# Kernel tuning notes

Hardware: AMD Instinct MI355X
Metric: run time of the kernel (lower is better)

The kernel has to match this reference:

```python
import jax, jax.numpy as jnp
import numpy as np

D = 512       # d_model
M = 64        # working memory_dim
SE = 32       # episodic slots
SS = 64       # semantic slots
H = 4         # episodic heads
B, L = 2, 1024
BOT = max(D // 4, 32)  # controller bottleneck = 128


def _layernorm(x, g, b, eps=1e-5):
    mu = jnp.mean(x, axis=-1, keepdims=True)
    var = jnp.var(x, axis=-1, keepdims=True)
    return (x - mu) * jax.lax.rsqrt(var + eps) * g + b


def setup_inputs() -> dict:
    key = jax.random.key(0)
    ks = jax.random.split(key, 24)
    r = lambda i, shape, s=0.02: jax.random.normal(ks[i], shape, dtype=jnp.float32) * s
    return {
        "x": jax.random.normal(ks[0], (B, L, D), dtype=jnp.float32),
        # WorkingMemory (weights stored as (in, out))
        "Wq": r(1, (D, M)), "Wk": r(2, (D, M)), "Wv": r(3, (D, D)),
        "Wf": r(4, (D, M)), "bf": jnp.zeros((M,), jnp.float32),
        "Wo": r(5, (D, D)),
        "ln_g": jnp.ones((D,), jnp.float32), "ln_b": jnp.zeros((D,), jnp.float32),
        # EpisodicMemory
        "eslots": r(6, (1, SE, D)),
        "Eq": r(7, (D, D)), "Ek": r(8, (D, D)), "Ev": r(9, (D, D)), "Eo": r(10, (D, D)),
        # SemanticMemory
        "know": r(11, (1, SS, D)),
        "Sin": r(12, (D, D)),
        "Sg_w": r(13, (D, D)), "Sg_b": jnp.zeros((D,), jnp.float32),
        "So": r(14, (D, D)),
        # MemoryController
        "C1w": r(15, (D, BOT)), "C1b": jnp.zeros((BOT,), jnp.float32),
        "C2w": r(16, (BOT, 3)), "C2b": jnp.zeros((3,), jnp.float32),
    }


def _forward(x, Wq, Wk, Wv, Wf, bf, Wo, ln_g, ln_b,
             eslots, Eq, Ek, Ev, Eo,
             know, Sin, Sg_w, Sg_b, So,
             C1w, C1b, C2w, C2b):
    b, l, d = x.shape
    # ---- WorkingMemory (parallel gated linear attention) ----
    scale = M ** -0.5
    q = (jax.nn.elu(x @ Wq) + 1.0) * scale          # (B,L,M)
    k = jax.nn.elu(x @ Wk) + 1.0                    # (B,L,M)
    v = x @ Wv                                      # (B,L,D)
    forget = jax.nn.sigmoid(x @ Wf + bf)            # (B,L,M)
    log_f_cum = jnp.clip(jnp.cumsum(jnp.log(jnp.clip(forget, 1e-6, None)), axis=1), -20.0, 20.0)
    exp_neg = jnp.exp(-log_f_cum)
    exp_pos = jnp.exp(log_f_cum)
    kv = k[..., :, None] * v[..., None, :]          # (B,L,M,D) outer product
    cum_kv = jnp.cumsum(exp_neg[..., None] * kv, axis=1)
    Mstate = exp_pos[..., None] * cum_kv            # (B,L,M,D)
    z = exp_pos * jnp.cumsum(exp_neg * k, axis=1)   # (B,L,M)
    num = jnp.einsum('blm,blmd->bld', q, Mstate)
    den = jnp.einsum('blm,blm->bl', q, z)[..., None] + 1e-6
    w_out = _layernorm(num / den, ln_g, ln_b) @ Wo  # (B,L,D)

    # ---- EpisodicMemory (cross-attn to learned slots) ----
    hd = D // H
    mem = jnp.broadcast_to(eslots, (b, SE, D))
    qh = (x @ Eq).reshape(b, l, H, hd)
    kh = (mem @ Ek).reshape(b, SE, H, hd)
    vh = (mem @ Ev).reshape(b, SE, H, hd)
    scores = jnp.einsum('blhe,bshe->bhls', qh, kh) / jnp.sqrt(jnp.float32(hd))
    attn = jax.nn.softmax(scores, axis=-1)
    e_out = jnp.einsum('bhls,bshe->blhe', attn, vh).reshape(b, l, D) @ Eo

    # ---- SemanticMemory (single-head attn to knowledge, gated residual) ----
    kb = jnp.broadcast_to(know, (b, SS, D))
    qs = x @ Sin                                    # (B,L,D)
    s_scores = jnp.einsum('bld,bsd->bls', qs, kb) / jnp.sqrt(jnp.float32(D))
    s_attn = jax.nn.softmax(s_scores, axis=-1)
    retrieved = jnp.einsum('bls,bsd->bld', s_attn, kb)
    gate = jax.nn.sigmoid(x @ Sg_w + Sg_b)
    s_out = (gate * retrieved + (1.0 - gate) * x) @ So

    # ---- Controller fusion ----
    wts = jax.nn.softmax(jax.nn.silu(x @ C1w + C1b) @ C2w + C2b, axis=-1)  # (B,L,3)
    fused = (wts[..., 0:1] * w_out + wts[..., 1:2] * e_out + wts[..., 2:3] * s_out)
    return fused


def reference(x, Wq, Wk, Wv, Wf, bf, Wo, ln_g, ln_b,
              eslots, Eq, Ek, Ev, Eo,
              know, Sin, Sg_w, Sg_b, So,
              C1w, C1b, C2w, C2b):
    return _forward(x, Wq, Wk, Wv, Wf, bf, Wo, ln_g, ln_b,
                    eslots, Eq, Ek, Ev, Eo,
                    know, Sin, Sg_w, Sg_b, So,
                    C1w, C1b, C2w, C2b)
```

## Files before the change

### kernel.cpp

```cpp
#include <hip/hip_runtime.h>
#include <cstdint>

typedef unsigned int uint;
typedef unsigned short ushort;
typedef __attribute__((ext_vector_type(8))) short bf16x8;
typedef __attribute__((ext_vector_type(4))) float f32x4;

__device__ __forceinline__ ushort f2b(float f) {
  union { float f; uint u; } v; v.f = f;
  uint u = v.u;
  uint r = (u + 0x7FFFu + ((u >> 16) & 1u)) >> 16;
  return (ushort)r;
}
__device__ __forceinline__ float b2f(ushort h) {
  union { uint u; float f; } v; v.u = ((uint)h) << 16; return v.f;
}

__global__ __launch_bounds__(256) void k_prep(
    const float* __restrict__ x, const float* __restrict__ Wv, const float* __restrict__ Sg,
    const float* __restrict__ C1w, const float* __restrict__ Wq, const float* __restrict__ Wk,
    const float* __restrict__ Wo, const float* __restrict__ So, const float* __restrict__ know,
    const float* __restrict__ eslots, const float* __restrict__ Ek, const float* __restrict__ Ev,
    const float* __restrict__ Sin, const float* __restrict__ Wf, const float* __restrict__ bfb,
    ushort* __restrict__ X16, ushort* __restrict__ Wcat, ushort* __restrict__ Wfin,
    ushort* __restrict__ know16, float* __restrict__ kh, float* __restrict__ vh,
    float* __restrict__ logfb)
{
  __shared__ __align__(16) float Af[16 * 32];
  __shared__ __align__(16) float Bf[32 * 64];
  __shared__ __align__(16) float T[64][65];
  int bid = blockIdx.x;
  int tid = threadIdx.x;
  int lane = tid & 63, wv = tid >> 6;

  if (bid < 128) {
    int r0 = bid * 16;
    int row = tid >> 4, col4 = (tid & 15) * 4;
    float a0 = 0.f, a1 = 0.f, a2 = 0.f, a3 = 0.f;
    for (int kt = 0; kt < 16; ++kt) {
      if (tid < 128) {
        int p = tid; int rr = p >> 3, c4 = (p & 7) * 4;
        *(float4*)&Af[rr * 32 + c4] = *(const float4*)&x[(size_t)(r0 + rr) * 512 + kt * 32 + c4];
      }
      #pragma unroll
      for (int i = 0; i < 2; ++i) {
        int p = i * 256 + tid; int rr = p >> 4, c4 = (p & 15) * 4;
        *(float4*)&Bf[rr * 64 + c4] = *(const float4*)&Wf[(size_t)(kt * 32 + rr) * 64 + c4];
      }
      __syncthreads();
      #pragma unroll 8
      for (int ks = 0; ks < 32; ++ks) {
        float a = Af[row * 32 + ks];
        float4 b = *(float4*)&Bf[ks * 64 + col4];
        a0 += a * b.x; a1 += a * b.y; a2 += a * b.z; a3 += a * b.w;
      }
      __syncthreads();
    }
    float accs[4] = {a0, a1, a2, a3};
    #pragma unroll
    for (int j = 0; j < 4; ++j) {
      float logit = accs[j] + bfb[col4 + j];
      float s = 1.f / (1.f + expf(-logit));
      logfb[(size_t)(r0 + row) * 64 + col4 + j] = logf(fmaxf(s, 1e-6f));
    }
    return;
  }
  if (bid < 256) {
    int t = (bid - 128) * 256 + tid;
    if (t < 16384) {
      int s = t >> 9, j = t & 511;
      float acc = 0.f;
      #pragma unroll 8
      for (int d = 0; d < 512; ++d) acc += eslots[s * 512 + d] * Ek[d * 512 + j];
      kh[s * 512 + j] = acc;
    } else {
      int o = t - 16384; int s = o >> 9, j = o & 511;
      float acc = 0.f;
      #pragma unroll 8
      for (int d = 0; d < 512; ++d) acc += eslots[s * 512 + d] * Ev[d * 512 + j];
      vh[s * 512 + j] = acc;
    }
    return;
  }
  if (bid < 384) {
    int k = (bid - 256) * 4 + wv;
    const float* sp = Sin + (size_t)k * 512 + lane * 8;
    float4 s1 = *(const float4*)&sp[0];
    float4 s2 = *(const float4*)&sp[4];
    for (int s = 0; s < 64; ++s) {
      const float* kp = know + (size_t)s * 512 + lane * 8;
      float4 k1 = *(const float4*)&kp[0];
      float4 k2 = *(const float4*)&kp[4];
      float part = s1.x * k1.x + s1.y * k1.y + s1.z * k1.z + s1.w * k1.w
                 + s2.x * k2.x + s2.y * k2.y + s2.z * k2.z + s2.w * k2.w;
      #pragma unroll
      for (int o = 32; o; o >>= 1) part += __shfl_xor(part, o);
      if (lane == 0) Wcat[(640 + s) * 512 + k] = f2b(part * 0.04419417382415922f);
    }
    return;
  }
  if (bid < 672) {
    int tt = bid - 384;
    const float* src; ushort* dst; int sld, dld, Nt, drow, dcol;
    if (tt < 64)       {           src = Wv;  dst = Wcat; sld = 512; dld = 512;  Nt = 8; drow = 0;    dcol = 0;   }
    else if (tt < 128) { tt -= 64; src = Sg;  dst = Wcat; sld = 512; dld = 512;  Nt = 8; drow = 704;  dcol = 0;   }
    else if (tt < 144) { tt -= 128; src = C1w; dst = Wcat; sld = 128; dld = 512; Nt = 2; drow = 1216; dcol = 0;   }
    else if (tt < 152) { tt -= 144; src = Wq;  dst = Wcat; sld = 64;  dld = 512; Nt = 1; drow = 1344; dcol = 0;   }
    else if (tt < 160) { tt -= 152; src = Wk;  dst = Wcat; sld = 64;  dld = 512; Nt = 1; drow = 1408; dcol = 0;   }
    else if (tt < 224) { tt -= 160; src = Wo;  dst = Wfin; sld = 512; dld = 1152; Nt = 8; drow = 0;   dcol = 0;   }
    else               { tt -= 224; src = So;  dst = Wfin; sld = 512; dld = 1152; Nt = 8; drow = 0;   dcol = 512; }
    int tk = tt / Nt, tn = tt % Nt;
    int k0 = tk * 64, n0 = tn * 64;
    int r = tid >> 4, c = (tid & 15) * 4;
    #pragma unroll
    for (int p = 0; p < 4; ++p) {
      int kk = p * 16 + r;
      float4 v = *(const float4*)&src[(size_t)(k0 + kk) * sld + n0 + c];
      T[c + 0][kk] = v.x; T[c + 1][kk] = v.y; T[c + 2][kk] = v.z; T[c + 3][kk] = v.w;
    }
    __syncthreads();
    int n = tid >> 2, kc = (tid & 3) * 16;
    uint u[8];
    #pragma unroll
    for (int j = 0; j < 8; ++j) {
      ushort lo = f2b(T[n][kc + 2 * j]);
      ushort hi = f2b(T[n][kc + 2 * j + 1]);
      u[j] = (uint)lo | ((uint)hi << 16);
    }
    size_t off = (size_t)(drow + n0 + n) * dld + dcol + k0 + kc;
    uint4 o1; o1.x = u[0]; o1.y = u[1]; o1.z = u[2]; o1.w = u[3];
    uint4 o2; o2.x = u[4]; o2.y = u[5]; o2.z = u[6]; o2.w = u[7];
    *(uint4*)&dst[off] = o1;
    *(uint4*)&dst[off + 8] = o2;
    return;
  }
  if (bid < 800) {
    int base = (bid - 672) * 256 + tid;
    #pragma unroll
    for (int it = 0; it < 8; ++it) {
      int t = base + it * 32768;
      float4 xv = *(const float4*)&x[(size_t)t * 4];
      uint2 o;
      o.x = (uint)f2b(xv.x) | ((uint)f2b(xv.y) << 16);
      o.y = (uint)f2b(xv.z) | ((uint)f2b(xv.w) << 16);
      *(uint2*)&X16[(size_t)t * 4] = o;
    }
    return;
  }
  {
    int t = (bid - 800) * 256 + tid;
    #pragma unroll
    for (int j = 0; j < 2; ++j) {
      float4 v = *(const float4*)&know[(size_t)t * 8 + j * 4];
      uint2 o;
      o.x = (uint)f2b(v.x) | ((uint)f2b(v.y) << 16);
      o.y = (uint)f2b(v.z) | ((uint)f2b(v.w) << 16);
      *(uint2*)&know16[(size_t)t * 8 + j * 4] = o;
    }
  }
}

__global__ __launch_bounds__(256) void k_pre2(
    const float* __restrict__ Eq, const float* __restrict__ kh, const float* __restrict__ vh,
    const float* __restrict__ Eo, ushort* __restrict__ Wcat, ushort* __restrict__ Wfin)
{
  int bid = blockIdx.x;
  int tid = threadIdx.x;
  int lane = tid & 63, wv = tid >> 6;
  if (bid < 256) {
    int gw = bid * 4 + wv;
    #pragma unroll
    for (int pp = 0; pp < 2; ++pp) {
      int pair = gw * 2 + pp;
      int k = pair >> 2, h = pair & 3;
      const float* ep = Eq + (size_t)k * 512 + h * 128 + lane * 2;
      float e0 = ep[0], e1 = ep[1];
      for (int s = 0; s < 32; ++s) {
        const float* kp = kh + (size_t)s * 512 + h * 128 + lane * 2;
        float part = e0 * kp[0] + e1 * kp[1];
        #pragma unroll
        for (int o = 32; o; o >>= 1) part += __shfl_xor(part, o);
        if (lane == 0) Wcat[(512 + h * 32 + s) * 512 + k] = f2b(part * 0.08838834764831845f);
      }
    }
  } else {
    int o = (bid - 256) * 256 + tid;
    int hs = o >> 9, j = o & 511;
    int h = hs >> 5, s = hs & 31;
    const float* vhp = vh + (size_t)s * 512 + h * 128;
    float acc = 0.f;
    #pragma unroll 8
    for (int e = 0; e < 128; ++e) acc += vhp[e] * Eo[(size_t)(h * 128 + e) * 512 + j];
    Wfin[(size_t)j * 1152 + 1024 + hs] = f2b(acc);
  }
}

__global__ __launch_bounds__(256) void k_gemm1(
    const ushort* __restrict__ A, const ushort* __restrict__ Bw, float* __restrict__ C,
    const float* __restrict__ sgb, const float* __restrict__ c1b)
{
  __shared__ __align__(16) ushort As[64 * 32];
  __shared__ __align__(16) ushort Bs[128 * 32];
  int tid = threadIdx.x;
  int lane = tid & 63, wv = tid >> 6;
  int wm = (wv & 1) * 32, wn = (wv >> 1) * 64;
  int lr = lane & 15, lk = lane >> 4;
  int m0 = blockIdx.y * 64, n0 = blockIdx.x * 128;
  f32x4 zero4 = {0.f, 0.f, 0.f, 0.f};
  f32x4 acc[2][4];
  #pragma unroll
  for (int a = 0; a < 2; ++a)
    #pragma unroll
    for (int b = 0; b < 4; ++b) acc[a][b] = zero4;
  for (int kt = 0; kt < 16; ++kt) {
    int k0 = kt * 32;
    {
      int p = tid, row = p >> 2, cc = p & 3;
      int cs = cc ^ ((row >> 1) & 3);
      *(uint4*)&As[p * 8] = *(const uint4*)&A[(size_t)(m0 + row) * 512 + k0 + cs * 8];
    }
    #pragma unroll
    for (int i = 0; i < 2; ++i) {
      int p = i * 256 + tid, row = p >> 2, cc = p & 3;
      int cs = cc ^ ((row >> 1) & 3);
      *(uint4*)&Bs[p * 8] = *(const uint4*)&Bw[(size_t)(n0 + row) * 512 + k0 + cs * 8];
    }
    __syncthreads();
    bf16x8 af[2], bfv[4];
    #pragma unroll
    for (int mi = 0; mi < 2; ++mi) {
      int row = wm + mi * 16 + lr;
      int cc = lk ^ ((row >> 1) & 3);
      af[mi] = *(bf16x8*)&As[row * 32 + cc * 8];
    }
    #pragma unroll
    for (int ni = 0; ni < 4; ++ni) {
      int row = wn + ni * 16 + lr;
      int cc = lk ^ ((row >> 1) & 3);
      bfv[ni] = *(bf16x8*)&Bs[row * 32 + cc * 8];
    }
    #pragma unroll
    for (int mi = 0; mi < 2; ++mi)
      #pragma unroll
      for (int ni = 0; ni < 4; ++ni)
        acc[mi][ni] = __builtin_amdgcn_mfma_f32_16x16x32_bf16(af[mi], bfv[ni], acc[mi][ni], 0, 0, 0);
    __syncthreads();
  }
  #pragma unroll
  for (int mi = 0; mi < 2; ++mi) {
    #pragma unroll
    for (int ni = 0; ni < 4; ++ni) {
      int col = n0 + wn + ni * 16 + lr;
      #pragma unroll
      for (int r = 0; r < 4; ++r) {
        int rowb = m0 + wm + mi * 16 + lk * 4 + r;
        float v = acc[mi][ni][r];
        if (col >= 704) {
          if (col < 1216) { v = 1.f / (1.f + __expf(-(v + sgb[col - 704]))); }
          else if (col < 1344) { float tt = v + c1b[col - 1216]; v = tt / (1.f + __expf(-tt)); }
          else if (col < 1408) { float e = (v > 0.f) ? v : (__expf(v) - 1.f); v = (e + 1.f) * 0.125f; }
          else if (col < 1472) { float e = (v > 0.f) ? v : (__expf(v) - 1.f); v = e + 1.f; }
        }
        C[(size_t)rowb * 1536 + col] = v;
      }
    }
  }
}

__global__ __launch_bounds__(256) void k_gemm2(
    const ushort* __restrict__ A, const ushort* __restrict__ Bw, float* __restrict__ C)
{
  __shared__ __align__(16) ushort As[64 * 32];
  __shared__ __align__(16) ushort Bs[64 * 32];
  int tid = threadIdx.x;
  int lane = tid & 63, wv = tid >> 6;
  int wm = (wv & 1) * 32, wn = (wv >> 1) * 32;
  int lr = lane & 15, lk = lane >> 4;
  int m0 = blockIdx.y * 64, n0 = blockIdx.x * 64;
  f32x4 zero4 = {0.f, 0.f, 0.f, 0.f};
  f32x4 acc[2][2];
  #pragma unroll
  for (int a = 0; a < 2; ++a)
    #pragma unroll
    for (int b = 0; b < 2; ++b) acc[a][b] = zero4;
  for (int kt = 0; kt < 36; ++kt) {
    int k0 = kt * 32;
    {
      int p = tid, row = p >> 2, cc = p & 3;
      int cs = cc ^ ((row >> 1) & 3);
      *(uint4*)&As[p * 8] = *(const uint4*)&A[(size_t)(m0 + row) * 1152 + k0 + cs * 8];
      *(uint4*)&Bs[p * 8] = *(const uint4*)&Bw[(size_t)(n0 + row) * 1152 + k0 + cs * 8];
    }
    __syncthreads();
    bf16x8 af[2], bfv[2];
    #pragma unroll
    for (int mi = 0; mi < 2; ++mi) {
      int row = wm + mi * 16 + lr;
      int cc = lk ^ ((row >> 1) & 3);
      af[mi] = *(bf16x8*)&As[row * 32 + cc * 8];
    }
    #pragma unroll
    for (int ni = 0; ni < 2; ++ni) {
      int row = wn + ni * 16 + lr;
      int cc = lk ^ ((row >> 1) & 3);
      bfv[ni] = *(bf16x8*)&Bs[row * 32 + cc * 8];
    }
    #pragma unroll
    for (int mi = 0; mi < 2; ++mi)
      #pragma unroll
      for (int ni = 0; ni < 2; ++ni)
        acc[mi][ni] = __builtin_amdgcn_mfma_f32_16x16x32_bf16(af[mi], bfv[ni], acc[mi][ni], 0, 0, 0);
    __syncthreads();
  }
  #pragma unroll
  for (int mi = 0; mi < 2; ++mi) {
    #pragma unroll
    for (int ni = 0; ni < 2; ++ni) {
      int col = n0 + wn + ni * 16 + lr;
      #pragma unroll
      for (int r = 0; r < 4; ++r) {
        int rowb = m0 + wm + mi * 16 + lk * 4 + r;
        C[(size_t)rowb * 512 + col] = acc[mi][ni][r];
      }
    }
  }
}

__global__ __launch_bounds__(256) void k_gatescan(
    const float* __restrict__ logfb, const float* __restrict__ P,
    float* __restrict__ cn, float* __restrict__ qe, float* __restrict__ qz)
{
  __shared__ float wsumA[4];
  __shared__ float wsumB[4];
  int bidx = blockIdx.x;
  int b = bidx >> 6, m = bidx & 63;
  int tid = threadIdx.x;
  int lane = tid & 63, wv = tid >> 6;
  size_t rbase = (size_t)b * 1024 + tid * 4;

  float v0 = logfb[(rbase + 0) * 64 + m];
  float v1 = logfb[(rbase + 1) * 64 + m];
  float v2 = logfb[(rbase + 2) * 64 + m];
  float v3 = logfb[(rbase + 3) * 64 + m];
  v1 += v0; v2 += v1; v3 += v2;
  float tsum = v3;
  float sc = tsum;
  #pragma unroll
  for (int o = 1; o < 64; o <<= 1) {
    float t = __shfl_up(sc, o, 64);
    if (lane >= o) sc += t;
  }
  if (lane == 63) wsumA[wv] = sc;
  __syncthreads();
  float excl = sc - tsum;
  #pragma unroll
  for (int w2 = 0; w2 < 3; ++w2) if (w2 < wv) excl += wsumA[w2];

  float vv[4] = {v0, v1, v2, v3};
  float cv[4], qv[4];
  #pragma unroll
  for (int i = 0; i < 4; ++i) {
    size_t r = rbase + i;
    float lf = fminf(fmaxf(excl + vv[i], -20.f), 20.f);
    float en = expf(-lf), ep = expf(lf);
    float kk = P[r * 1536 + 1408 + m];
    float qq = P[r * 1536 + 1344 + m];
    cv[i] = en * kk;
    qv[i] = qq * ep;
    cn[r * 64 + m] = cv[i];
    qe[r * 64 + m] = qv[i];
  }

  float c1 = cv[0], c2 = c1 + cv[1], c3 = c2 + cv[2], c4 = c3 + cv[3];
  float t2 = c4;
  float sc2 = t2;
  #pragma unroll
  for (int o = 1; o < 64; o <<= 1) {
    float t = __shfl_up(sc2, o, 64);
    if (lane >= o) sc2 += t;
  }
  if (lane == 63) wsumB[wv] = sc2;
  __syncthreads();
  float excl2 = sc2 - t2;
  #pragma unroll
  for (int w2 = 0; w2 < 3; ++w2) if (w2 < wv) excl2 += wsumB[w2];

  float pr[4] = {c1, c2, c3, c4};
  #pragma unroll
  for (int i = 0; i < 4; ++i) {
    size_t r = rbase + i;
    qz[r * 64 + m] = qv[i] * (excl2 + pr[i]);
  }
}

__global__ __launch_bounds__(256) void k_scanA(
    const float* __restrict__ cn, const float* __restrict__ P, float* __restrict__ Send)
{
  __shared__ __align__(16) float cnS[16 * 64];
  __shared__ __align__(16) float vS[16 * 64];
  int tid = threadIdx.x;
  int bid = blockIdx.x;
  int dt = bid & 7, c = (bid >> 3) & 15, b = bid >> 7;
  int rb0 = b * 1024 + c * 64;
  int mg = tid >> 4, dl = tid & 15;
  float4 acc[4];
  #pragma unroll
  for (int i = 0; i < 4; ++i) acc[i] = make_float4(0.f, 0.f, 0.f, 0.f);
  for (int ig = 0; ig < 4; ++ig) {
    int rb = rb0 + ig * 16;
    int row = tid >> 4, c4f = (tid & 15) * 4;
    *(float4*)&cnS[row * 64 + c4f] = *(const float4*)&cn[(size_t)(rb + row) * 64 + c4f];
    *(float4*)&vS[row * 64 + c4f] = *(const float4*)&P[(size_t)(rb + row) * 1536 + dt * 64 + c4f];
    __syncthreads();
    #pragma unroll 4
    for (int i = 0; i < 16; ++i) {
      float4 vv = *(float4*)&vS[i * 64 + dl * 4];
      float4 cm = *(float4*)&cnS[i * 64 + mg * 4];
      acc[0].x += cm.x * vv.x; acc[0].y += cm.x * vv.y; acc[0].z += cm.x * vv.z; acc[0].w += cm.x * vv.w;
      acc[1].x += cm.y * vv.x; acc[1].y += cm.y * vv.y; acc[1].z += cm.y * vv.z; acc[1].w += cm.y * vv.w;
      acc[2].x += cm.z * vv.x; acc[2].y += cm.z * vv.y; acc[2].z += cm.z * vv.z; acc[2].w += cm.z * vv.w;
      acc[3].x += cm.w * vv.x; acc[3].y += cm.w * vv.y; acc[3].z += cm.w * vv.z; acc[3].w += cm.w * vv.w;
    }
    __syncthreads();
  }
  #pragma unroll
  for (int mi = 0; mi < 4; ++mi) {
    int m = mg * 4 + mi;
    *(float4*)&Send[(size_t)((b * 16 + c) * 64 + m) * 512 + dt * 64 + dl * 4] = acc[mi];
  }
}

__global__ __launch_bounds__(256) void k_scanB(const float* __restrict__ Send, float* __restrict__ carry)
{
  int t = blockIdx.x * 256 + threadIdx.x;
  int d = t & 511, m = (t >> 9) & 63, b = t >> 15;
  float run = 0.f;
  for (int c = 0; c < 16; ++c) {
    size_t idx = (size_t)((b * 16 + c) * 64 + m) * 512 + d;
    carry[idx] = run;
    run += Send[idx];
  }
}

__global__ __launch_bounds__(256) void k_scanC(
    const float* __restrict__ cn, const float* __restrict__ qe, const float* __restrict__ P,
    const float* __restrict__ carry, float* __restrict__ num)
{
  __shared__ __align__(16) float cnS[16 * 64];
  __shared__ __align__(16) float qeS[16 * 64];
  __shared__ __align__(16) float vS[16 * 64];
  int tid = threadIdx.x;
  int bid = blockIdx.x;
  int dt = bid & 7, c = (bid >> 3) & 15, b = bid >> 7;
  int rb0 = b * 1024 + c * 64;
  int mg = tid & 3, dl = tid >> 2;
  int d = dt * 64 + dl;
  float S[16];
  #pragma unroll
  for (int mi = 0; mi < 16; ++mi)
    S[mi] = carry[(size_t)((b * 16 + c) * 64 + mg * 16 + mi) * 512 + d];
  for (int ig = 0; ig < 4; ++ig) {
    int rb = rb0 + ig * 16;
    int row = tid >> 4, c4f = (tid & 15) * 4;
    *(float4*)&cnS[row * 64 + c4f] = *(const float4*)&cn[(size_t)(rb + row) * 64 + c4f];
    *(float4*)&qeS[row * 64 + c4f] = *(const float4*)&qe[(size_t)(rb + row) * 64 + c4f];
    *(float4*)&vS[row * 64 + c4f] = *(const float4*)&P[(size_t)(rb + row) * 1536 + dt * 64 + c4f];
    __syncthreads();
    for (int i = 0; i < 16; ++i) {
      float vv = vS[i * 64 + dl];
      float p = 0.f;
      #pragma unroll
      for (int j = 0; j < 4; ++j) {
        float4 c4 = *(float4*)&cnS[i * 64 + mg * 16 + j * 4];
        float4 q4 = *(float4*)&qeS[i * 64 + mg * 16 + j * 4];
        S[j * 4 + 0] += c4.x * vv; p += q4.x * S[j * 4 + 0];
        S[j * 4 + 1] += c4.y * vv; p += q4.y * S[j * 4 + 1];
        S[j * 4 + 2] += c4.z * vv; p += q4.z * S[j * 4 + 2];
        S[j * 4 + 3] += c4.w * vv; p += q4.w * S[j * 4 + 3];
      }
      p += __shfl_xor(p, 1);
      p += __shfl_xor(p, 2);
      if (mg == 0) num[(size_t)(rb + i) * 512 + d] = p;
    }
    __syncthreads();
  }
}

__global__ __launch_bounds__(256) void k_post(
    const float* __restrict__ P, const float* __restrict__ x,
    const float* __restrict__ num, const float* __restrict__ qz,
    const ushort* __restrict__ know16, const float* __restrict__ lng,
    const float* __restrict__ lnb, const float* __restrict__ C2w,
    const float* __restrict__ C2b, ushort* __restrict__ Afin)
{
  __shared__ __align__(16) ushort kbuf[32 * 512];
  __shared__ float attnL[4][64];
  __shared__ float w2L[4];
  int tid = threadIdx.x;
  int w = tid >> 6, lane = tid & 63;
  int r0 = blockIdx.x * 4;
  int r = r0 + w;
  size_t pr = (size_t)r * 1536;

  float h0 = P[pr + 1216 + lane], h1 = P[pr + 1280 + lane];
  float a0 = h0 * C2w[lane * 3 + 0] + h1 * C2w[(64 + lane) * 3 + 0];
  float a1 = h0 * C2w[lane * 3 + 1] + h1 * C2w[(64 + lane) * 3 + 1];
  float a2 = h0 * C2w[lane * 3 + 2] + h1 * C2w[(64 + lane) * 3 + 2];
  #pragma unroll
  for (int o = 32; o; o >>= 1) {
    a0 += __shfl_xor(a0, o); a1 += __shfl_xor(a1, o); a2 += __shfl_xor(a2, o);
  }
  a0 += C2b[0]; a1 += C2b[1]; a2 += C2b[2];
  float mxc = fmaxf(a0, fmaxf(a1, a2));
  float e0 = expf(a0 - mxc), e1 = expf(a1 - mxc), e2c = expf(a2 - mxc);
  float inv = 1.f / (e0 + e1 + e2c);
  float w0 = e0 * inv, w1 = e1 * inv, w2 = e2c * inv;
  if (lane == 0) w2L[w] = w2;

  {
    float den = qz[(size_t)r * 64 + lane];
    #pragma unroll
    for (int o = 32; o; o >>= 1) den += __shfl_xor(den, o);
    den += 1e-6f;
    float y[8];
    float4 n0 = *(const float4*)&num[(size_t)r * 512 + lane * 8];
    float4 n1 = *(const float4*)&num[(size_t)r * 512 + lane * 8 + 4];
    y[0] = n0.x / den; y[1] = n0.y / den; y[2] = n0.z / den; y[3] = n0.w / den;
    y[4] = n1.x / den; y[5] = n1.y / den; y[6] = n1.z / den; y[7] = n1.w / den;
    float s1 = 0.f, s2 = 0.f;
    #pragma unroll
    for (int i = 0; i < 8; ++i) { s1 += y[i]; s2 += y[i] * y[i]; }
    #pragma unroll
    for (int o = 32; o; o >>= 1) { s1 += __shfl_xor(s1, o); s2 += __shfl_xor(s2, o); }
    float mu = s1 * (1.f / 512.f);
    float var = s2 * (1.f / 512.f) - mu * mu;
    float rs = rsqrtf(var + 1e-5f);
    uint4 outv;
    uint pk[4];
    #pragma unroll
    for (int p2 = 0; p2 < 4; ++p2) {
      float o0 = (y[2 * p2] - mu) * rs * lng[lane * 8 + 2 * p2] + lnb[lane * 8 + 2 * p2];
      float o1 = (y[2 * p2 + 1] - mu) * rs * lng[lane * 8 + 2 * p2 + 1] + lnb[lane * 8 + 2 * p2 + 1];
      pk[p2] = (uint)f2b(o0 * w0) | ((uint)f2b(o1 * w0) << 16);
    }
    outv.x = pk[0]; outv.y = pk[1]; outv.z = pk[2]; outv.w = pk[3];
    *(uint4*)&Afin[(size_t)r * 1152 + lane * 8] = outv;
  }

  {
    int h = lane >> 4, ei = (lane & 15) * 2;
    float v0 = P[pr + 512 + h * 32 + ei], v1 = P[pr + 512 + h * 32 + ei + 1];
    float mxe = fmaxf(v0, v1);
    #pragma unroll
    for (int o = 1; o < 16; o <<= 1) mxe = fmaxf(mxe, __shfl_xor(mxe, o));
    float ee0 = __expf(v0 - mxe), ee1 = __expf(v1 - mxe);
    float ss = ee0 + ee1;
    #pragma unroll
    for (int o = 1; o < 16; o <<= 1) ss += __shfl_xor(ss, o);
    float sc1 = w1 / ss;
    uint pkv = (uint)f2b(ee0 * sc1) | ((uint)f2b(ee1 * sc1) << 16);
    *(uint*)&Afin[(size_t)r * 1152 + 1024 + h * 32 + ei] = pkv;
  }

  {
    float lv = P[pr + 640 + lane];
    float mx = lv;
    #pragma unroll
    for (int o = 32; o; o >>= 1) mx = fmaxf(mx, __shfl_xor(mx, o));
    float e = __expf(lv - mx);
    float sum = e;
    #pragma unroll
    for (int o = 32; o; o >>= 1) sum += __shfl_xor(sum, o);
    attnL[w][lane] = e / sum;
  }

  int dd = tid * 2;
  float acc[4][2];
  #pragma unroll
  for (int i = 0; i < 4; ++i) { acc[i][0] = 0.f; acc[i][1] = 0.f; }
  for (int hs = 0; hs < 2; ++hs) {
    #pragma unroll
    for (int i = 0; i < 8; ++i) {
      int idx = i * 256 + tid;
      *(uint4*)&kbuf[idx * 8] = *(const uint4*)&know16[(size_t)hs * 16384 + idx * 8];
    }
    __syncthreads();
    for (int s = 0; s < 32; ++s) {
      uint uu = *(uint*)&kbuf[s * 512 + dd];
      float k0 = b2f((ushort)(uu & 0xffff));
      float k1 = b2f((ushort)(uu >> 16));
      #pragma unroll
      for (int row = 0; row < 4; ++row) {
        float a = attnL[row][hs * 32 + s];
        acc[row][0] += a * k0;
        acc[row][1] += a * k1;
      }
    }
    __syncthreads();
  }
  #pragma unroll
  for (int row = 0; row < 4; ++row) {
    int rr = r0 + row;
    float g0 = P[(size_t)rr * 1536 + 704 + dd];
    float g1 = P[(size_t)rr * 1536 + 704 + dd + 1];
    float x0 = x[(size_t)rr * 512 + dd], x1 = x[(size_t)rr * 512 + dd + 1];
    float w2v = w2L[row];
    float m0 = g0 * acc[row][0] + (1.f - g0) * x0;
    float m1 = g1 * acc[row][1] + (1.f - g1) * x1;
    uint pkv = (uint)f2b(w2v * m0) | ((uint)f2b(w2v * m1) << 16);
    *(uint*)&Afin[(size_t)rr * 1152 + 512 + dd] = pkv;
  }
}

extern "C" void kernel_launch(void* const* d_in, const int* in_sizes, int n_in,
                              void* d_out, int out_size, void* d_ws, size_t ws_size,
                              hipStream_t stream)
{
  const float* x     = (const float*)d_in[0];
  const float* Wq    = (const float*)d_in[1];
  const float* Wk    = (const float*)d_in[2];
  const float* Wv    = (const float*)d_in[3];
  const float* Wf    = (const float*)d_in[4];
  const float* bfb   = (const float*)d_in[5];
  const float* Wo    = (const float*)d_in[6];
  const float* ln_g  = (const float*)d_in[7];
  const float* ln_b  = (const float*)d_in[8];
  const float* eslots= (const float*)d_in[9];
  const float* Eq    = (const float*)d_in[10];
  const float* Ek    = (const float*)d_in[11];
  const float* Ev    = (const float*)d_in[12];
  const float* Eo    = (const float*)d_in[13];
  const float* know  = (const float*)d_in[14];
  const float* Sin   = (const float*)d_in[15];
  const float* Sg_w  = (const float*)d_in[16];
  const float* Sg_b  = (const float*)d_in[17];
  const float* So    = (const float*)d_in[18];
  const float* C1w   = (const float*)d_in[19];
  const float* C1b   = (const float*)d_in[20];
  const float* C2w   = (const float*)d_in[21];
  const float* C2b   = (const float*)d_in[22];

  char* ws = (char*)d_ws;
  ushort* X16    = (ushort*)(ws + 0);
  ushort* Wcat   = (ushort*)(ws + 2097152);
  ushort* Wfin   = (ushort*)(ws + 3670016);
  ushort* know16 = (ushort*)(ws + 4849664);
  float*  kh     = (float*)(ws + 4915200);
  float*  vh     = (float*)(ws + 4980736);
  float*  P      = (float*)(ws + 5046272);
  float*  logfb  = (float*)(ws + 17629184);
  float*  cn     = (float*)(ws + 18153472);
  float*  qe     = (float*)(ws + 18677760);
  float*  qz     = (float*)(ws + 19202048);
  float*  Send   = (float*)(ws + 19726336);
  float*  carry  = (float*)(ws + 23920640);
  float*  num    = (float*)(ws + 28114944);
  ushort* Afin   = (ushort*)(ws + 32342016);

  k_prep<<<dim3(816), dim3(256), 0, stream>>>(x, Wv, Sg_w, C1w, Wq, Wk, Wo, So, know,
                                              eslots, Ek, Ev, Sin, Wf, bfb,
                                              X16, Wcat, Wfin, know16, kh, vh, logfb);
  k_pre2<<<dim3(512), dim3(256), 0, stream>>>(Eq, kh, vh, Eo, Wcat, Wfin);
  k_gemm1<<<dim3(12, 32), dim3(256), 0, stream>>>(X16, Wcat, P, Sg_b, C1b);
  k_gatescan<<<dim3(128), dim3(256), 0, stream>>>(logfb, P, cn, qe, qz);
  k_scanA<<<dim3(256), dim3(256), 0, stream>>>(cn, P, Send);
  k_scanB<<<dim3(256), dim3(256), 0, stream>>>(Send, carry);
  k_scanC<<<dim3(256), dim3(256), 0, stream>>>(cn, qe, P, carry, num);
  k_post<<<dim3(512), dim3(256), 0, stream>>>(P, x, num, qz, know16, ln_g, ln_b, C2w, C2b, Afin);
  k_gemm2<<<dim3(8, 32), dim3(256), 0, stream>>>(Afin, Wfin, (float*)d_out);
}
```

Baseline: 145.3 us.

## Halve scan chunk length to double scan blocks and restructure prep gate matmul

The chunked linear-attention scan now uses 32-row chunks instead of 64, doubling the block count of scanA/scanC to 512 and lengthening the serial carry loop in scanB to 32 steps. cn/qe tiles are loaded once per block rather than per subtile, and workspace offsets grow to fit the larger Send/carry buffers. The forget-gate matmul in k_prep now stages whole x rows in a shared pool and reads Wf straight from global memory. A missing __syncthreads in k_post before attnL is consumed is also added, which fixes a possible race.

```diff
diff --git a/kernel.cpp b/kernel.cpp
--- a/kernel.cpp
+++ b/kernel.cpp
@@ -26,42 +26,35 @@
     ushort* __restrict__ know16, float* __restrict__ kh, float* __restrict__ vh,
     float* __restrict__ logfb)
 {
-  __shared__ __align__(16) float Af[16 * 32];
-  __shared__ __align__(16) float Bf[32 * 64];
-  __shared__ __align__(16) float T[64][65];
+  __shared__ __align__(16) float pool[8320];
   int bid = blockIdx.x;
   int tid = threadIdx.x;
   int lane = tid & 63, wv = tid >> 6;
 
   if (bid < 128) {
+    float* xS = pool;
     int r0 = bid * 16;
-    int row = tid >> 4, col4 = (tid & 15) * 4;
+    #pragma unroll
+    for (int it = 0; it < 8; ++it) {
+      int p = it * 256 + tid;
+      int rr = p >> 7, c4 = (p & 127) * 4;
+      *(float4*)&xS[rr * 512 + c4] = *(const float4*)&x[(size_t)(r0 + rr) * 512 + c4];
+    }
+    __syncthreads();
+    int row = tid >> 4, c4 = (tid & 15) * 4;
     float a0 = 0.f, a1 = 0.f, a2 = 0.f, a3 = 0.f;
-    for (int kt = 0; kt < 16; ++kt) {
-      if (tid < 128) {
-        int p = tid; int rr = p >> 3, c4 = (p & 7) * 4;
-        *(float4*)&Af[rr * 32 + c4] = *(const float4*)&x[(size_t)(r0 + rr) * 512 + kt * 32 + c4];
-      }
-      #pragma unroll
-      for (int i = 0; i < 2; ++i) {
-        int p = i * 256 + tid; int rr = p >> 4, c4 = (p & 15) * 4;
-        *(float4*)&Bf[rr * 64 + c4] = *(const float4*)&Wf[(size_t)(kt * 32 + rr) * 64 + c4];
-      }
-      __syncthreads();
-      #pragma unroll 8
-      for (int ks = 0; ks < 32; ++ks) {
-        float a = Af[row * 32 + ks];
-        float4 b = *(float4*)&Bf[ks * 64 + col4];
-        a0 += a * b.x; a1 += a * b.y; a2 += a * b.z; a3 += a * b.w;
-      }
-      __syncthreads();
+    #pragma unroll 8
+    for (int d = 0; d < 512; ++d) {
+      float a = xS[row * 512 + d];
+      float4 w = *(const float4*)&Wf[(size_t)d * 64 + c4];
+      a0 += a * w.x; a1 += a * w.y; a2 += a * w.z; a3 += a * w.w;
     }
     float accs[4] = {a0, a1, a2, a3};
     #pragma unroll
     for (int j = 0; j < 4; ++j) {
-      float logit = accs[j] + bfb[col4 + j];
+      float logit = accs[j] + bfb[c4 + j];
       float s = 1.f / (1.f + expf(-logit));
-      logfb[(size_t)(r0 + row) * 64 + col4 + j] = logf(fmaxf(s, 1e-6f));
+      logfb[(size_t)(r0 + row) * 64 + c4 + j] = logf(fmaxf(s, 1e-6f));
     }
     return;
   }
@@ -100,6 +93,7 @@
     return;
   }
   if (bid < 672) {
+    #define Tm(a,b) pool[(a) * 65 + (b)]
     int tt = bid - 384;
     const float* src; ushort* dst; int sld, dld, Nt, drow, dcol;
     if (tt < 64)       {           src = Wv;  dst = Wcat; sld = 512; dld = 512;  Nt = 8; drow = 0;    dcol = 0;   }
@@ -116,15 +110,15 @@
     for (int p = 0; p < 4; ++p) {
       int kk = p * 16 + r;
       float4 v = *(const float4*)&src[(size_t)(k0 + kk) * sld + n0 + c];
-      T[c + 0][kk] = v.x; T[c + 1][kk] = v.y; T[c + 2][kk] = v.z; T[c + 3][kk] = v.w;
+      Tm(c + 0, kk) = v.x; Tm(c + 1, kk) = v.y; Tm(c + 2, kk) = v.z; Tm(c + 3, kk) = v.w;
     }
     __syncthreads();
     int n = tid >> 2, kc = (tid & 3) * 16;
     uint u[8];
     #pragma unroll
     for (int j = 0; j < 8; ++j) {
-      ushort lo = f2b(T[n][kc + 2 * j]);
-      ushort hi = f2b(T[n][kc + 2 * j + 1]);
+      ushort lo = f2b(Tm(n, kc + 2 * j));
+      ushort hi = f2b(Tm(n, kc + 2 * j + 1));
       u[j] = (uint)lo | ((uint)hi << 16);
     }
     size_t off = (size_t)(drow + n0 + n) * dld + dcol + k0 + kc;
@@ -132,6 +126,7 @@
     uint4 o2; o2.x = u[4]; o2.y = u[5]; o2.z = u[6]; o2.w = u[7];
     *(uint4*)&dst[off] = o1;
     *(uint4*)&dst[off + 8] = o2;
+    #undef Tm
     return;
   }
   if (bid < 800) {
@@ -396,26 +391,32 @@
 __global__ __launch_bounds__(256) void k_scanA(
     const float* __restrict__ cn, const float* __restrict__ P, float* __restrict__ Send)
 {
-  __shared__ __align__(16) float cnS[16 * 64];
+  __shared__ __align__(16) float cnS[32 * 64];
   __shared__ __align__(16) float vS[16 * 64];
   int tid = threadIdx.x;
   int bid = blockIdx.x;
-  int dt = bid & 7, c = (bid >> 3) & 15, b = bid >> 7;
-  int rb0 = b * 1024 + c * 64;
+  int dt = bid & 7, c = (bid >> 3) & 31, b = bid >> 8;
+  int rb0 = b * 1024 + c * 32;
+  #pragma unroll
+  for (int it = 0; it < 2; ++it) {
+    int p = it * 256 + tid;
+    int row = p >> 4, c4f = (p & 15) * 4;
+    *(float4*)&cnS[row * 64 + c4f] = *(const float4*)&cn[(size_t)(rb0 + row) * 64 + c4f];
+  }
+  __syncthreads();
   int mg = tid >> 4, dl = tid & 15;
   float4 acc[4];
   #pragma unroll
   for (int i = 0; i < 4; ++i) acc[i] = make_float4(0.f, 0.f, 0.f, 0.f);
-  for (int ig = 0; ig < 4; ++ig) {
+  for (int ig = 0; ig < 2; ++ig) {
     int rb = rb0 + ig * 16;
     int row = tid >> 4, c4f = (tid & 15) * 4;
-    *(float4*)&cnS[row * 64 + c4f] = *(const float4*)&cn[(size_t)(rb + row) * 64 + c4f];
     *(float4*)&vS[row * 64 + c4f] = *(const float4*)&P[(size_t)(rb + row) * 1536 + dt * 64 + c4f];
     __syncthreads();
     #pragma unroll 4
     for (int i = 0; i < 16; ++i) {
       float4 vv = *(float4*)&vS[i * 64 + dl * 4];
-      float4 cm = *(float4*)&cnS[i * 64 + mg * 4];
+      float4 cm = *(float4*)&cnS[(ig * 16 + i) * 64 + mg * 4];
       acc[0].x += cm.x * vv.x; acc[0].y += cm.x * vv.y; acc[0].z += cm.x * vv.z; acc[0].w += cm.x * vv.w;
       acc[1].x += cm.y * vv.x; acc[1].y += cm.y * vv.y; acc[1].z += cm.y * vv.z; acc[1].w += cm.y * vv.w;
       acc[2].x += cm.z * vv.x; acc[2].y += cm.z * vv.y; acc[2].z += cm.z * vv.z; acc[2].w += cm.z * vv.w;
@@ -426,7 +427,7 @@
   #pragma unroll
   for (int mi = 0; mi < 4; ++mi) {
     int m = mg * 4 + mi;
-    *(float4*)&Send[(size_t)((b * 16 + c) * 64 + m) * 512 + dt * 64 + dl * 4] = acc[mi];
+    *(float4*)&Send[(size_t)((b * 32 + c) * 64 + m) * 512 + dt * 64 + dl * 4] = acc[mi];
   }
 }
 
@@ -435,8 +436,8 @@
   int t = blockIdx.x * 256 + threadIdx.x;
   int d = t & 511, m = (t >> 9) & 63, b = t >> 15;
   float run = 0.f;
-  for (int c = 0; c < 16; ++c) {
-    size_t idx = (size_t)((b * 16 + c) * 64 + m) * 512 + d;
+  for (int c = 0; c < 32; ++c) {
+    size_t idx = (size_t)((b * 32 + c) * 64 + m) * 512 + d;
     carry[idx] = run;
     run += Send[idx];
   }
@@ -446,33 +447,40 @@
     const float* __restrict__ cn, const float* __restrict__ qe, const float* __restrict__ P,
     const float* __restrict__ carry, float* __restrict__ num)
 {
-  __shared__ __align__(16) float cnS[16 * 64];
-  __shared__ __align__(16) float qeS[16 * 64];
+  __shared__ __align__(16) float cnS[32 * 64];
+  __shared__ __align__(16) float qeS[32 * 64];
   __shared__ __align__(16) float vS[16 * 64];
   int tid = threadIdx.x;
   int bid = blockIdx.x;
-  int dt = bid & 7, c = (bid >> 3) & 15, b = bid >> 7;
-  int rb0 = b * 1024 + c * 64;
+  int dt = bid & 7, c = (bid >> 3) & 31, b = bid >> 8;
+  int rb0 = b * 1024 + c * 32;
+  #pragma unroll
+  for (int it = 0; it < 2; ++it) {
+    int p = it * 256 + tid;
+    int row = p >> 4, c4f = (p & 15) * 4;
+    *(float4*)&cnS[row * 64 + c4f] = *(const float4*)&cn[(size_t)(rb0 + row) * 64 + c4f];
+    *(float4*)&qeS[row * 64 + c4f] = *(const float4*)&qe[(size_t)(rb0 + row) * 64 + c4f];
+  }
   int mg = tid & 3, dl = tid >> 2;
   int d = dt * 64 + dl;
   float S[16];
   #pragma unroll
   for (int mi = 0; mi < 16; ++mi)
-    S[mi] = carry[(size_t)((b * 16 + c) * 64 + mg * 16 + mi) * 512 + d];
-  for (int ig = 0; ig < 4; ++ig) {
+    S[mi] = carry[(size_t)((b * 32 + c) * 64 + mg * 16 + mi) * 512 + d];
+  __syncthreads();
+  for (int ig = 0; ig < 2; ++ig) {
     int rb = rb0 + ig * 16;
     int row = tid >> 4, c4f = (tid & 15) * 4;
-    *(float4*)&cnS[row * 64 + c4f] = *(const float4*)&cn[(size_t)(rb + row) * 64 + c4f];
-    *(float4*)&qeS[row * 64 + c4f] = *(const float4*)&qe[(size_t)(rb + row) * 64 + c4f];
     *(float4*)&vS[row * 64 + c4f] = *(const float4*)&P[(size_t)(rb + row) * 1536 + dt * 64 + c4f];
     __syncthreads();
     for (int i = 0; i < 16; ++i) {
+      int ii = ig * 16 + i;
       float vv = vS[i * 64 + dl];
       float p = 0.f;
       #pragma unroll
       for (int j = 0; j < 4; ++j) {
-        float4 c4 = *(float4*)&cnS[i * 64 + mg * 16 + j * 4];
-        float4 q4 = *(float4*)&qeS[i * 64 + mg * 16 + j * 4];
+        float4 c4 = *(float4*)&cnS[ii * 64 + mg * 16 + j * 4];
+        float4 q4 = *(float4*)&qeS[ii * 64 + mg * 16 + j * 4];
         S[j * 4 + 0] += c4.x * vv; p += q4.x * S[j * 4 + 0];
         S[j * 4 + 1] += c4.y * vv; p += q4.y * S[j * 4 + 1];
         S[j * 4 + 2] += c4.z * vv; p += q4.z * S[j * 4 + 2];
@@ -480,7 +488,7 @@
       }
       p += __shfl_xor(p, 1);
       p += __shfl_xor(p, 2);
-      if (mg == 0) num[(size_t)(rb + i) * 512 + d] = p;
+      if (mg == 0) num[(size_t)(rb0 + ii) * 512 + d] = p;
     }
     __syncthreads();
   }
@@ -573,6 +581,7 @@
     for (int o = 32; o; o >>= 1) sum += __shfl_xor(sum, o);
     attnL[w][lane] = e / sum;
   }
+  __syncthreads();
 
   int dd = tid * 2;
   float acc[4][2];
@@ -653,9 +662,9 @@
   float*  qe     = (float*)(ws + 18677760);
   float*  qz     = (float*)(ws + 19202048);
   float*  Send   = (float*)(ws + 19726336);
-  float*  carry  = (float*)(ws + 23920640);
-  float*  num    = (float*)(ws + 28114944);
-  ushort* Afin   = (ushort*)(ws + 32342016);
+  float*  carry  = (float*)(ws + 28114944);
+  float*  num    = (float*)(ws + 36503552);
+  ushort* Afin   = (ushort*)(ws + 40697856);
 
   k_prep<<<dim3(816), dim3(256), 0, stream>>>(x, Wv, Sg_w, C1w, Wq, Wk, Wo, So, know,
                                               eslots, Ek, Ev, Sin, Wf, bfb,
@@ -663,9 +672,9 @@
   k_pre2<<<dim3(512), dim3(256), 0, stream>>>(Eq, kh, vh, Eo, Wcat, Wfin);
   k_gemm1<<<dim3(12, 32), dim3(256), 0, stream>>>(X16, Wcat, P, Sg_b, C1b);
   k_gatescan<<<dim3(128), dim3(256), 0, stream>>>(logfb, P, cn, qe, qz);
-  k_scanA<<<dim3(256), dim3(256), 0, stream>>>(cn, P, Send);
+  k_scanA<<<dim3(512), dim3(256), 0, stream>>>(cn, P, Send);
   k_scanB<<<dim3(256), dim3(256), 0, stream>>>(Send, carry);
-  k_scanC<<<dim3(256), dim3(256), 0, stream>>>(cn, qe, P, carry, num);
+  k_scanC<<<dim3(512), dim3(256), 0, stream>>>(cn, qe, P, carry, num);
   k_post<<<dim3(512), dim3(256), 0, stream>>>(P, x, num, qz, know16, ln_g, ln_b, C2w, C2b, Afin);
   k_gemm2<<<dim3(8, 32), dim3(256), 0, stream>>>(Afin, Wfin, (float*)d_out);
 }
```

Result: faster. 142.0 us (-2.2%).
